# Kernel tuning notes

Measured on AMD Instinct MI355X. Metric: run time of the kernel, lower is better.

## Reference

```python
import jax, jax.numpy as jnp
import numpy as np

K = 7          # involution kernel size
G = 16         # groups = channels // group_channels = 256 // 16
BN_EPS = 1e-3  # Keras BatchNormalization default epsilon


def setup_inputs() -> dict:
    key = jax.random.key(0)
    ks = jax.random.split(key, 6)
    B, H, W, C = 4, 56, 56, 256
    Cr = C // 4                      # reduction_ratio = 4
    x = jax.random.normal(ks[0], (B, H, W, C), dtype=jnp.float32)
    w_reduce = jax.random.normal(ks[1], (C, Cr), dtype=jnp.float32) * (1.0 / np.sqrt(C))
    gamma = jnp.ones((Cr,), dtype=jnp.float32)
    beta = jnp.zeros((Cr,), dtype=jnp.float32)
    mean = jax.random.normal(ks[2], (Cr,), dtype=jnp.float32) * 0.1
    var = jax.random.uniform(ks[3], (Cr,), dtype=jnp.float32) + 0.5
    w_span = jax.random.normal(ks[4], (Cr, K * K * G), dtype=jnp.float32) * (1.0 / np.sqrt(Cr))
    b_span = jnp.zeros((K * K * G,), dtype=jnp.float32)
    return {"x": x, "w_reduce": w_reduce, "gamma": gamma, "beta": beta,
            "mean": mean, "var": var, "w_span": w_span, "b_span": b_span}


def reference(x, w_reduce, gamma, beta, mean, var, w_span, b_span):
    B, H, W, C = x.shape
    Cg = C // G  # channels per group
    # kernel generation branch: 1x1 conv -> BN (inference) -> ReLU -> 1x1 conv
    r = jnp.einsum('bhwc,cd->bhwd', x, w_reduce)
    r = jax.nn.relu((r - mean) * (gamma / jnp.sqrt(var + BN_EPS)) + beta)
    kgen = jnp.einsum('bhwd,de->bhwe', r, w_span) + b_span      # (B,H,W,K*K*G)
    kgen = kgen.reshape(B, H, W, G, K * K)
    # im2col with SAME padding (stride=1, pad (K-1)//2 symmetric), depth order (kh, kw, C)
    p = (K - 1) // 2
    xp = jnp.pad(x, ((0, 0), (p, p), (p, p), (0, 0)))
    patches = jnp.stack([xp[:, i:i + H, j:j + W, :]
                         for i in range(K) for j in range(K)], axis=3)  # (B,H,W,K*K,C)
    patches = patches.reshape(B, H, W, K * K, G, Cg)
    # per-pixel, per-group weighted reduction over the K*K window
    out = jnp.einsum('bhwgk,bhwkgc->bhwgc', kgen, patches)
    return out.reshape(B, H, W, C)
```

## Files before the change

kernel.cpp:

```cpp
#include <hip/hip_runtime.h>
#include <hip/hip_bf16.h>
#include <stdint.h>

#define B_   4
#define H_   56
#define W_   56
#define C_   256
#define CR   64
#define G_   16
#define CG   16
#define KS   7
#define KK   49
#define PADR 3
#define NPX  (B_*H_*W_)

typedef __attribute__((ext_vector_type(8))) short bf16x8;
typedef __attribute__((ext_vector_type(4))) float f32x4;
typedef __attribute__((ext_vector_type(2))) float f32x2;

__device__ __forceinline__ uint32_t f2bf(float f) {
    uint32_t x = __float_as_uint(f);
    return (x + 0x7fffu + ((x >> 16) & 1u)) >> 16;
}
__device__ __forceinline__ uint32_t pkbf(float a, float b) {
    union { __hip_bfloat162 h; uint32_t u; } c;
    c.h = __float22bfloat162_rn(make_float2(a, b));
    return c.u;
}
__device__ __forceinline__ float blo(uint32_t w) { return __uint_as_float(w << 16); }
__device__ __forceinline__ float bhi(uint32_t w) { return __uint_as_float(w & 0xffff0000u); }

union U4V { uint4 u; bf16x8 v; };

__global__ __launch_bounds__(256) void k1_reduce(
        const float* __restrict__ x, const float* __restrict__ wreduce,
        const float* __restrict__ wspan,
        const float* __restrict__ gamma, const float* __restrict__ beta,
        const float* __restrict__ mean, const float* __restrict__ var,
        uint16_t* __restrict__ r, uint16_t* __restrict__ wpp) {
    __shared__ __align__(16) uint16_t wrpLds[16384];
    int tid = threadIdx.x;
    int lane = tid & 63, w = tid >> 6;

    #pragma unroll
    for (int q = 0; q < 8; ++q) {
        int f  = q * 256 + tid;
        int fl = f & 63, nb = (f >> 6) & 3, kb = f >> 8;
        int k0 = kb * 32 + (fl >> 4) * 8;
        int n  = nb * 16 + (fl & 15);
        uint32_t wd[4];
        #pragma unroll
        for (int jj = 0; jj < 4; ++jj)
            wd[jj] = pkbf(wreduce[(k0 + 2 * jj) * CR + n],
                          wreduce[(k0 + 2 * jj + 1) * CR + n]);
        *(uint4*)(wrpLds + f * 8) = make_uint4(wd[0], wd[1], wd[2], wd[3]);
    }
    if (blockIdx.x < 128 && tid < 64) {
        int f  = blockIdx.x * 64 + tid;
        int fl = f & 63, nb = (f >> 6) & 3, kb = (f >> 8) & 1, g = f >> 9;
        int k0 = kb * 32 + (fl >> 4) * 8;
        int n  = nb * 16 + (fl & 15);
        uint32_t wd[4];
        #pragma unroll
        for (int jj = 0; jj < 4; ++jj) {
            float a = (n < KK) ? wspan[(k0 + 2 * jj) * (KK * G_) + g * KK + n] : 0.f;
            float c = (n < KK) ? wspan[(k0 + 2 * jj + 1) * (KK * G_) + g * KK + n] : 0.f;
            wd[jj] = pkbf(a, c);
        }
        *(uint4*)(wpp + (size_t)f * 8) = make_uint4(wd[0], wd[1], wd[2], wd[3]);
    }
    __syncthreads();

    int mt  = blockIdx.x * 4 + w;
    int pix = mt * 16 + (lane & 15);
    int ko  = (lane >> 4) * 8;
    const float* xrow = x + (size_t)pix * C_ + ko;
    f32x4 acc[4] = {{0,0,0,0},{0,0,0,0},{0,0,0,0},{0,0,0,0}};
    #pragma unroll
    for (int kb = 0; kb < 8; ++kb) {
        float4 a0 = *(const float4*)(xrow + kb * 32);
        float4 a1 = *(const float4*)(xrow + kb * 32 + 4);
        U4V af;
        af.u = make_uint4(pkbf(a0.x, a0.y), pkbf(a0.z, a0.w),
                          pkbf(a1.x, a1.y), pkbf(a1.z, a1.w));
        const uint16_t* wb = wrpLds + kb * 2048 + lane * 8;
        #pragma unroll
        for (int nb = 0; nb < 4; ++nb) {
            bf16x8 bf_ = *(const bf16x8*)(wb + nb * 512);
            acc[nb] = __builtin_amdgcn_mfma_f32_16x16x32_bf16(af.v, bf_, acc[nb], 0, 0, 0);
        }
    }
    int rq = (lane >> 4) * 4;
    #pragma unroll
    for (int nb = 0; nb < 4; ++nb) {
        int d = nb * 16 + (lane & 15);
        float s  = gamma[d] * rsqrtf(var[d] + 1e-3f);
        float sh = beta[d] - mean[d] * s;
        #pragma unroll
        for (int rg = 0; rg < 4; ++rg) {
            float v = fmaf(acc[nb][rg], s, sh);
            v = v > 0.f ? v : 0.f;
            r[(size_t)(mt * 16 + rq + rg) * CR + d] = (uint16_t)f2bf(v);
        }
    }
}

#define TS   14
#define HS   20
#define XSP  21
#define KGW  56

__global__ __launch_bounds__(256, 4) void k2_involution(
        const float* __restrict__ x, const uint16_t* __restrict__ r,
        const uint16_t* __restrict__ wpp, const float* __restrict__ bspan,
        float* __restrict__ out) {
    __shared__ __align__(16) uint16_t xs[420 * 16];
    __shared__ __align__(16) uint16_t kg[196 * KGW];

    int tid  = threadIdx.x;
    int tile = blockIdx.x, g = blockIdx.y, b = blockIdx.z;
    int ty0 = (tile >> 2) * TS, tx0 = (tile & 3) * TS;

    #pragma unroll
    for (int pass = 0; pass < 2; ++pass) {
        int i = tid + pass * 256;
        if (i < HS * HS) {
            int py = i / HS, px = i % HS;
            int gy = ty0 + py - PADR, gx = tx0 + px - PADR;
            uint4 wA = make_uint4(0, 0, 0, 0), wB = wA;
            if (gy >= 0 && gy < H_ && gx >= 0 && gx < W_) {
                const float* xp = x + (((size_t)(b * H_ + gy)) * W_ + gx) * C_ + g * CG;
                float4 a0 = *(const float4*)(xp);
                float4 a1 = *(const float4*)(xp + 4);
                float4 a2 = *(const float4*)(xp + 8);
                float4 a3 = *(const float4*)(xp + 12);
                wA = make_uint4(pkbf(a0.x, a0.y), pkbf(a0.z, a0.w),
                                pkbf(a1.x, a1.y), pkbf(a1.z, a1.w));
                wB = make_uint4(pkbf(a2.x, a2.y), pkbf(a2.z, a2.w),
                                pkbf(a3.x, a3.y), pkbf(a3.z, a3.w));
            }
            uint16_t* dst = xs + (py * XSP + px) * 16;
            *(uint4*)(dst + 0) = wA;
            *(uint4*)(dst + 8) = wB;
        }
    }

    int lane = tid & 63, w = tid >> 6;
    bf16x8 bfr[2][4];
    const uint16_t* wb = wpp + g * 4096 + lane * 8;
    #pragma unroll
    for (int kb = 0; kb < 2; ++kb)
        #pragma unroll
        for (int nb = 0; nb < 4; ++nb)
            bfr[kb][nb] = *(const bf16x8*)(wb + kb * 2048 + nb * 512);
    float bias[4];
    #pragma unroll
    for (int nb = 0; nb < 4; ++nb) {
        int n = nb * 16 + (lane & 15);
        bias[nb] = (n < KK) ? bspan[g * KK + n] : 0.f;
    }
    for (int mi = 0; mi < 4; ++mi) {
        int mt = mi * 4 + w;
        if (mt < 13) {
            int m  = mt * 16 + (lane & 15);
            int mm = m < 196 ? m : 195;
            int ly = mm / TS, lx = mm % TS;
            size_t pix = ((size_t)(b * H_ + ty0 + ly)) * W_ + (tx0 + lx);
            const uint16_t* rp = r + pix * CR + (lane >> 4) * 8;
            bf16x8 a0 = *(const bf16x8*)(rp);
            bf16x8 a1 = *(const bf16x8*)(rp + 32);
            f32x4 acc[4];
            #pragma unroll
            for (int nb = 0; nb < 4; ++nb)
                acc[nb] = (f32x4){bias[nb], bias[nb], bias[nb], bias[nb]};
            #pragma unroll
            for (int nb = 0; nb < 4; ++nb) {
                acc[nb] = __builtin_amdgcn_mfma_f32_16x16x32_bf16(a0, bfr[0][nb], acc[nb], 0, 0, 0);
                acc[nb] = __builtin_amdgcn_mfma_f32_16x16x32_bf16(a1, bfr[1][nb], acc[nb], 0, 0, 0);
            }
            int row = mt * 16 + (lane >> 4) * 4;
            if (row < 196) {
                #pragma unroll
                for (int nb = 0; nb < 4; ++nb) {
                    int n = nb * 16 + (lane & 15);
                    if (n < KK) {
                        int slot = n + n / 7;
                        #pragma unroll
                        for (int rg = 0; rg < 4; ++rg) {
                            int rr  = row + rg;
                            int rho = (rr >> 1) + (rr & 1) * 98;
                            kg[rho * KGW + slot] = (uint16_t)f2bf(acc[nb][rg]);
                        }
                    }
                }
            }
        }
    }
    __syncthreads();

    if (tid < 196) {
        int p = tid >> 1, h = tid & 1;
        int ty = p / 7, tx = (p % 7) * 2;
        const uint16_t* kgL = kg + p * KGW;
        const uint16_t* kgR = kg + (98 + p) * KGW;

        f32x2 accL[4] = {{0,0},{0,0},{0,0},{0,0}};
        f32x2 accR[4] = {{0,0},{0,0},{0,0},{0,0}};
        #pragma unroll
        for (int kh = 0; kh < KS; ++kh) {
            uint4 aL = *(const uint4*)(kgL + kh * 8);
            uint4 aR = *(const uint4*)(kgR + kh * 8);
            const uint32_t kwL[4] = {aL.x, aL.y, aL.z, aL.w};
            const uint32_t kwR[4] = {aR.x, aR.y, aR.z, aR.w};
            const uint16_t* xrow = xs + ((ty + kh) * XSP + tx) * 16 + h * 8;
            #pragma unroll
            for (int j = 0; j < 8; ++j) {
                uint4 xw = *(const uint4*)(xrow + j * 16);
                f32x2 x0 = {blo(xw.x), bhi(xw.x)};
                f32x2 x1 = {blo(xw.y), bhi(xw.y)};
                f32x2 x2 = {blo(xw.z), bhi(xw.z)};
                f32x2 x3 = {blo(xw.w), bhi(xw.w)};
                if (j < 7) {
                    float kv = (j & 1) ? bhi(kwL[j >> 1]) : blo(kwL[j >> 1]);
                    f32x2 kL = {kv, kv};
                    accL[0] = __builtin_elementwise_fma(kL, x0, accL[0]);
                    accL[1] = __builtin_elementwise_fma(kL, x1, accL[1]);
                    accL[2] = __builtin_elementwise_fma(kL, x2, accL[2]);
                    accL[3] = __builtin_elementwise_fma(kL, x3, accL[3]);
                }
                if (j > 0) {
                    int t = j - 1;
                    float kv = (t & 1) ? bhi(kwR[t >> 1]) : blo(kwR[t >> 1]);
                    f32x2 kR = {kv, kv};
                    accR[0] = __builtin_elementwise_fma(kR, x0, accR[0]);
                    accR[1] = __builtin_elementwise_fma(kR, x1, accR[1]);
                    accR[2] = __builtin_elementwise_fma(kR, x2, accR[2]);
                    accR[3] = __builtin_elementwise_fma(kR, x3, accR[3]);
                }
            }
        }
        size_t pixL = ((size_t)(b * H_ + ty0 + ty)) * W_ + (tx0 + tx);
        float* opL = out + pixL * C_ + g * CG + h * 8;
        float* opR = opL + C_;
        *(float4*)(opL + 0) = make_float4(accL[0].x, accL[0].y, accL[1].x, accL[1].y);
        *(float4*)(opL + 4) = make_float4(accL[2].x, accL[2].y, accL[3].x, accL[3].y);
        *(float4*)(opR + 0) = make_float4(accR[0].x, accR[0].y, accR[1].x, accR[1].y);
        *(float4*)(opR + 4) = make_float4(accR[2].x, accR[2].y, accR[3].x, accR[3].y);
    }
}

extern "C" void kernel_launch(void* const* d_in, const int* in_sizes, int n_in,
                              void* d_out, int out_size, void* d_ws, size_t ws_size,
                              hipStream_t stream) {
    const float* x        = (const float*)d_in[0];
    const float* w_reduce = (const float*)d_in[1];
    const float* gamma    = (const float*)d_in[2];
    const float* beta     = (const float*)d_in[3];
    const float* mean     = (const float*)d_in[4];
    const float* var      = (const float*)d_in[5];
    const float* w_span   = (const float*)d_in[6];
    const float* b_span   = (const float*)d_in[7];
    float* out = (float*)d_out;

    uint8_t* ws = (uint8_t*)d_ws;
    uint16_t* r_ws = (uint16_t*)(ws + 0);
    uint16_t* wpp  = (uint16_t*)(ws + 1605632);

    hipLaunchKernelGGL(k1_reduce, dim3(NPX / 64), dim3(256), 0, stream,
                       x, w_reduce, w_span, gamma, beta, mean, var, r_ws, wpp);
    hipLaunchKernelGGL(k2_involution, dim3(16, 16, B_), dim3(256), 0, stream,
                       x, r_ws, wpp, b_span, out);
}
```

Baseline: 102.9 us.

## Fuse reduce GEMM into involution kernel and prepack weights in separate kernel

Moves the 1x1 reduce conv plus BN/ReLU into the involution kernel, computing r per tile into swizzled LDS instead of round-tripping through global memory. Weight packing and BN scale/shift are split into a small prepack kernel. Each group block now recomputes the full reduction for its tile, so the reduce GEMM and x reads are repeated across the 16 groups. Occupancy drops to 2 blocks per CU due to larger LDS.

```diff
diff --git a/kernel.cpp b/kernel.cpp
--- a/kernel.cpp
+++ b/kernel.cpp
@@ -32,76 +32,31 @@
 
 union U4V { uint4 u; bf16x8 v; };
 
-__global__ __launch_bounds__(256) void k1_reduce(
-        const float* __restrict__ x, const float* __restrict__ wreduce,
-        const float* __restrict__ wspan,
+__global__ __launch_bounds__(256) void k0_prepack(
+        const float* __restrict__ wr, const float* __restrict__ wspan,
         const float* __restrict__ gamma, const float* __restrict__ beta,
         const float* __restrict__ mean, const float* __restrict__ var,
-        uint16_t* __restrict__ r, uint16_t* __restrict__ wpp) {
-    __shared__ __align__(16) uint16_t wrpLds[16384];
-    int tid = threadIdx.x;
-    int lane = tid & 63, w = tid >> 6;
-
-    #pragma unroll
-    for (int q = 0; q < 8; ++q) {
-        int f  = q * 256 + tid;
-        int fl = f & 63, nb = (f >> 6) & 3, kb = f >> 8;
-        int k0 = kb * 32 + (fl >> 4) * 8;
-        int n  = nb * 16 + (fl & 15);
-        uint32_t wd[4];
-        #pragma unroll
-        for (int jj = 0; jj < 4; ++jj)
-            wd[jj] = pkbf(wreduce[(k0 + 2 * jj) * CR + n],
-                          wreduce[(k0 + 2 * jj + 1) * CR + n]);
-        *(uint4*)(wrpLds + f * 8) = make_uint4(wd[0], wd[1], wd[2], wd[3]);
-    }
-    if (blockIdx.x < 128 && tid < 64) {
-        int f  = blockIdx.x * 64 + tid;
-        int fl = f & 63, nb = (f >> 6) & 3, kb = (f >> 8) & 1, g = f >> 9;
-        int k0 = kb * 32 + (fl >> 4) * 8;
-        int n  = nb * 16 + (fl & 15);
-        uint32_t wd[4];
-        #pragma unroll
-        for (int jj = 0; jj < 4; ++jj) {
-            float a = (n < KK) ? wspan[(k0 + 2 * jj) * (KK * G_) + g * KK + n] : 0.f;
-            float c = (n < KK) ? wspan[(k0 + 2 * jj + 1) * (KK * G_) + g * KK + n] : 0.f;
-            wd[jj] = pkbf(a, c);
-        }
-        *(uint4*)(wpp + (size_t)f * 8) = make_uint4(wd[0], wd[1], wd[2], wd[3]);
-    }
-    __syncthreads();
-
-    int mt  = blockIdx.x * 4 + w;
-    int pix = mt * 16 + (lane & 15);
-    int ko  = (lane >> 4) * 8;
-    const float* xrow = x + (size_t)pix * C_ + ko;
-    f32x4 acc[4] = {{0,0,0,0},{0,0,0,0},{0,0,0,0},{0,0,0,0}};
-    #pragma unroll
-    for (int kb = 0; kb < 8; ++kb) {
-        float4 a0 = *(const float4*)(xrow + kb * 32);
-        float4 a1 = *(const float4*)(xrow + kb * 32 + 4);
-        U4V af;
-        af.u = make_uint4(pkbf(a0.x, a0.y), pkbf(a0.z, a0.w),
-                          pkbf(a1.x, a1.y), pkbf(a1.z, a1.w));
-        const uint16_t* wb = wrpLds + kb * 2048 + lane * 8;
-        #pragma unroll
-        for (int nb = 0; nb < 4; ++nb) {
-            bf16x8 bf_ = *(const bf16x8*)(wb + nb * 512);
-            acc[nb] = __builtin_amdgcn_mfma_f32_16x16x32_bf16(af.v, bf_, acc[nb], 0, 0, 0);
-        }
-    }
-    int rq = (lane >> 4) * 4;
-    #pragma unroll
-    for (int nb = 0; nb < 4; ++nb) {
-        int d = nb * 16 + (lane & 15);
-        float s  = gamma[d] * rsqrtf(var[d] + 1e-3f);
-        float sh = beta[d] - mean[d] * s;
-        #pragma unroll
-        for (int rg = 0; rg < 4; ++rg) {
-            float v = fmaf(acc[nb][rg], s, sh);
-            v = v > 0.f ? v : 0.f;
-            r[(size_t)(mt * 16 + rq + rg) * CR + d] = (uint16_t)f2bf(v);
-        }
+        uint16_t* __restrict__ wrp, uint16_t* __restrict__ wpp,
+        float* __restrict__ scale, float* __restrict__ shift) {
+    int idx = blockIdx.x * 256 + threadIdx.x;
+    {
+        int j = idx & 7, lane = (idx >> 3) & 63, nb = (idx >> 9) & 3,
+            kb = (idx >> 11) & 1, g = idx >> 12;
+        int k = kb * 32 + (lane >> 4) * 8 + j;
+        int n = nb * 16 + (lane & 15);
+        float v = (n < KK) ? wspan[k * (KK * G_) + g * KK + n] : 0.f;
+        wpp[idx] = (uint16_t)f2bf(v);
+    }
+    if (idx < 16384) {
+        int j = idx & 7, lane = (idx >> 3) & 63, nb = (idx >> 9) & 3, kb = idx >> 11;
+        int k = kb * 32 + (lane >> 4) * 8 + j;
+        int n = nb * 16 + (lane & 15);
+        wrp[idx] = (uint16_t)f2bf(wr[k * CR + n]);
+    }
+    if (idx < CR) {
+        float s = gamma[idx] * rsqrtf(var[idx] + 1e-3f);
+        scale[idx] = s;
+        shift[idx] = beta[idx] - mean[idx] * s;
     }
 }
 
@@ -110,16 +65,26 @@
 #define XSP  21
 #define KGW  56
 
-__global__ __launch_bounds__(256, 4) void k2_involution(
-        const float* __restrict__ x, const uint16_t* __restrict__ r,
-        const uint16_t* __restrict__ wpp, const float* __restrict__ bspan,
-        float* __restrict__ out) {
-    __shared__ __align__(16) uint16_t xs[420 * 16];
-    __shared__ __align__(16) uint16_t kg[196 * KGW];
+#define LDS_XS   0
+#define LDS_WK   13440
+#define LDS_RB   (13440 + 32768)
+#define LDS_TOT  (13440 + 32768 + 25088)
+
+__global__ __launch_bounds__(256, 2) void k_fused(
+        const float* __restrict__ x, const uint16_t* __restrict__ wrp,
+        const uint16_t* __restrict__ wpp,
+        const float* __restrict__ scale, const float* __restrict__ shift,
+        const float* __restrict__ bspan, float* __restrict__ out) {
+    __shared__ __align__(16) uint8_t lds[LDS_TOT];
+    uint16_t* xs   = (uint16_t*)(lds + LDS_XS);
+    uint16_t* wrpL = (uint16_t*)(lds + LDS_WK);
+    uint16_t* kg   = (uint16_t*)(lds + LDS_WK);
+    uint8_t*  rb   = lds + LDS_RB;
 
     int tid  = threadIdx.x;
     int tile = blockIdx.x, g = blockIdx.y, b = blockIdx.z;
     int ty0 = (tile >> 2) * TS, tx0 = (tile & 3) * TS;
+    int lane = tid & 63, w = tid >> 6;
 
     #pragma unroll
     for (int pass = 0; pass < 2; ++pass) {
@@ -144,31 +109,84 @@
             *(uint4*)(dst + 8) = wB;
         }
     }
-
-    int lane = tid & 63, w = tid >> 6;
+    #pragma unroll
+    for (int q = 0; q < 8; ++q) {
+        int f = q * 256 + tid;
+        *(uint4*)(wrpL + f * 8) = *(const uint4*)(wrp + f * 8);
+    }
+    __syncthreads();
+
+    int rq = (lane >> 4) * 4;
+    float s16[16], sh16[16];
+    #pragma unroll
+    for (int mtc = 0; mtc < 4; ++mtc)
+        #pragma unroll
+        for (int rg = 0; rg < 4; ++rg) {
+            int ch = mtc * 16 + rq + rg;
+            s16[mtc * 4 + rg]  = scale[ch];
+            sh16[mtc * 4 + rg] = shift[ch];
+        }
+    for (int nt = w; nt < 13; nt += 4) {
+        int m  = nt * 16 + (lane & 15);
+        int mm = m < 196 ? m : 195;
+        int ly = mm / TS, lx = mm % TS;
+        size_t pix = ((size_t)(b * H_ + ty0 + ly)) * W_ + (tx0 + lx);
+        const float* xrow = x + pix * C_ + (lane >> 4) * 8;
+        f32x4 acc[4] = {{0,0,0,0},{0,0,0,0},{0,0,0,0},{0,0,0,0}};
+        #pragma unroll
+        for (int kb = 0; kb < 8; ++kb) {
+            float4 a0 = *(const float4*)(xrow + kb * 32);
+            float4 a1 = *(const float4*)(xrow + kb * 32 + 4);
+            U4V xf;
+            xf.u = make_uint4(pkbf(a0.x, a0.y), pkbf(a0.z, a0.w),
+                              pkbf(a1.x, a1.y), pkbf(a1.z, a1.w));
+            const uint16_t* wbase = wrpL + kb * 2048 + lane * 8;
+            #pragma unroll
+            for (int mtc = 0; mtc < 4; ++mtc) {
+                bf16x8 af = *(const bf16x8*)(wbase + mtc * 512);
+                acc[mtc] = __builtin_amdgcn_mfma_f32_16x16x32_bf16(af, xf.v, acc[mtc], 0, 0, 0);
+            }
+        }
+        if (m < 196) {
+            #pragma unroll
+            for (int mtc = 0; mtc < 4; ++mtc) {
+                float v0 = fmaf(acc[mtc][0], s16[mtc*4+0], sh16[mtc*4+0]); v0 = v0 > 0.f ? v0 : 0.f;
+                float v1 = fmaf(acc[mtc][1], s16[mtc*4+1], sh16[mtc*4+1]); v1 = v1 > 0.f ? v1 : 0.f;
+                float v2 = fmaf(acc[mtc][2], s16[mtc*4+2], sh16[mtc*4+2]); v2 = v2 > 0.f ? v2 : 0.f;
+                float v3 = fmaf(acc[mtc][3], s16[mtc*4+3], sh16[mtc*4+3]); v3 = v3 > 0.f ? v3 : 0.f;
+                int c2  = mtc * 32 + rq * 2;
+                int blk = c2 >> 4, within = c2 & 15;
+                uint32_t off = (uint32_t)m * 128 + (((blk ^ (m & 7)) << 4) | within);
+                *(uint2*)(rb + off) = make_uint2(pkbf(v0, v1), pkbf(v2, v3));
+            }
+        }
+    }
+
     bf16x8 bfr[2][4];
-    const uint16_t* wb = wpp + g * 4096 + lane * 8;
+    const uint16_t* wb2 = wpp + g * 4096 + lane * 8;
     #pragma unroll
     for (int kb = 0; kb < 2; ++kb)
         #pragma unroll
         for (int nb = 0; nb < 4; ++nb)
-            bfr[kb][nb] = *(const bf16x8*)(wb + kb * 2048 + nb * 512);
+            bfr[kb][nb] = *(const bf16x8*)(wb2 + kb * 2048 + nb * 512);
     float bias[4];
     #pragma unroll
     for (int nb = 0; nb < 4; ++nb) {
         int n = nb * 16 + (lane & 15);
         bias[nb] = (n < KK) ? bspan[g * KK + n] : 0.f;
     }
+    __syncthreads();
+
     for (int mi = 0; mi < 4; ++mi) {
         int mt = mi * 4 + w;
         if (mt < 13) {
             int m  = mt * 16 + (lane & 15);
             int mm = m < 196 ? m : 195;
-            int ly = mm / TS, lx = mm % TS;
-            size_t pix = ((size_t)(b * H_ + ty0 + ly)) * W_ + (tx0 + lx);
-            const uint16_t* rp = r + pix * CR + (lane >> 4) * 8;
-            bf16x8 a0 = *(const bf16x8*)(rp);
-            bf16x8 a1 = *(const bf16x8*)(rp + 32);
+            int q  = lane >> 4;
+            uint32_t offA = (uint32_t)mm * 128 + (uint32_t)(((q     ^ (mm & 7)) << 4));
+            uint32_t offB = (uint32_t)mm * 128 + (uint32_t)((((4+q) ^ (mm & 7)) << 4));
+            bf16x8 a0 = *(const bf16x8*)(rb + offA);
+            bf16x8 a1 = *(const bf16x8*)(rb + offB);
             f32x4 acc[4];
             #pragma unroll
             for (int nb = 0; nb < 4; ++nb)
@@ -263,11 +281,14 @@
     float* out = (float*)d_out;
 
     uint8_t* ws = (uint8_t*)d_ws;
-    uint16_t* r_ws = (uint16_t*)(ws + 0);
-    uint16_t* wpp  = (uint16_t*)(ws + 1605632);
-
-    hipLaunchKernelGGL(k1_reduce, dim3(NPX / 64), dim3(256), 0, stream,
-                       x, w_reduce, w_span, gamma, beta, mean, var, r_ws, wpp);
-    hipLaunchKernelGGL(k2_involution, dim3(16, 16, B_), dim3(256), 0, stream,
-                       x, r_ws, wpp, b_span, out);
-}
+    uint16_t* wrp   = (uint16_t*)(ws + 0);
+    uint16_t* wpp   = (uint16_t*)(ws + 32768);
+    float*    scale = (float*)   (ws + 163840);
+    float*    shift = (float*)   (ws + 164096);
+
+    hipLaunchKernelGGL(k0_prepack, dim3(256), dim3(256), 0, stream,
+                       w_reduce, w_span, gamma, beta, mean, var,
+                       wrp, wpp, scale, shift);
+    hipLaunchKernelGGL(k_fused, dim3(16, 16, B_), dim3(256), 0, stream,
+                       x, wrp, wpp, scale, shift, b_span, out);
+}
```

Result: slower. 118.3 us (+15.0%).
